# Kernel tuning notes

Measured on AMD Instinct MI355X. Metric: run time of the kernel, lower is better.

## Reference

```python
import jax, jax.numpy as jnp
import numpy as np

# --- static anchor geometry (exactly mirrors RPN._make_anchor_box) ---

def _valid_idx():
    scales = [64.0, 128.0, 256.0]
    ratios = [0.5, 1.0, 2.0]
    # (h, w) per anchor, normalized by 448
    anc = np.array([[s / np.sqrt(r), s * np.sqrt(r)] for s in scales for r in ratios]) / 448.0
    c = (np.arange(28) + 0.5) / 28.0
    cy = np.repeat(c, 28).reshape(28, 28)  # y varies along rows
    cx = np.tile(c, (28, 1))               # x varies along cols
    boxes = np.zeros((28, 28, 36))
    for a in range(9):
        boxes[..., 4 * a + 0] = cy
        boxes[..., 4 * a + 1] = cx
        boxes[..., 4 * a + 2] = anc[a, 0]
        boxes[..., 4 * a + 3] = anc[a, 1]
    b = boxes.reshape(-1, 4)  # [7056, 4] in yxhw
    y1 = b[:, 0] - b[:, 2] / 2
    x1 = b[:, 1] - b[:, 3] / 2
    y2 = b[:, 0] + b[:, 2] / 2
    x2 = b[:, 1] + b[:, 3] / 2
    return np.where((y1 > 0) & (x1 > 0) & (y2 < 28) & (x2 < 28))[0]

_VALID = _valid_idx()  # 4850 static indices

ROI_CLS_THRESHOLD = 0.9


def setup_inputs() -> dict:
    key = jax.random.key(0)
    ks = jax.random.split(key, 4)
    C = 2048
    return {
        'x': jax.random.normal(ks[0], (1, C, 28, 28), jnp.float32),
        'conv_w': jax.random.normal(ks[1], (C, C, 3, 3), jnp.float32) * 0.02,
        'conv_b': jnp.zeros((C,), jnp.float32),
        'reg_w': jax.random.normal(ks[2], (36, C), jnp.float32) * 0.02,
        'reg_b': jnp.zeros((36,), jnp.float32),
        'cls_w': jax.random.normal(ks[3], (9, C), jnp.float32) * 0.02,
        'cls_b': jnp.zeros((9,), jnp.float32),
    }


def reference(x, conv_w, conv_b, reg_w, reg_b, cls_w, cls_b):
    # Conv block: 3x3 conv + BatchNorm(identity at init: gamma=1, beta=0, running stats 0/1) + ReLU
    h = jax.lax.conv_general_dilated(
        x, conv_w, window_strides=(1, 1), padding=((1, 1), (1, 1)),
        dimension_numbers=('NCHW', 'OIHW', 'NCHW'))
    h = jax.nn.relu(h + conv_b[None, :, None, None])
    # 1x1 conv heads + sigmoid
    reg = jax.nn.sigmoid(jnp.einsum('bchw,oc->bohw', h, reg_w) + reg_b[None, :, None, None])  # [1,36,28,28]
    cls = jax.nn.sigmoid(jnp.einsum('bchw,oc->bohw', h, cls_w) + cls_b[None, :, None, None])  # [1,9,28,28]
    # exact replication of view/permute/squeeze + static valid-anchor gather
    reg = reg.reshape(1, 4, -1).transpose(0, 2, 1)[0][_VALID]  # [4850, 4]
    cls = cls.reshape(-1)[_VALID]                              # [4850]
    # inference path (gt=None): reg[cls > 0.9]; fixed-shape masked equivalent
    keep = cls > ROI_CLS_THRESHOLD
    return reg * keep[:, None]
```

## Files before the change

### kernel.cpp

```cpp
#include <hip/hip_runtime.h>
#include <cstdint>

typedef __attribute__((ext_vector_type(8))) short s8v;
typedef __attribute__((ext_vector_type(4))) float f4v;

__device__ __forceinline__ unsigned short bf16_rne(float f) {
    unsigned u = __float_as_uint(f);
    u += 0x7FFFu + ((u >> 16) & 1u);
    return (unsigned short)(u >> 16);
}
__device__ __forceinline__ float bf16f(unsigned short h) {
    return __uint_as_float(((unsigned)h) << 16);
}
__device__ __forceinline__ void cvt2(float a, float b, unsigned& hiw, unsigned& low) {
    unsigned ua = __float_as_uint(a), ub = __float_as_uint(b);
    unsigned ha = ua + 0x7FFFu + ((ua >> 16) & 1u);
    unsigned hb = ub + 0x7FFFu + ((ub >> 16) & 1u);
    hiw = (ha >> 16) | (hb & 0xFFFF0000u);
    float ra = a - __uint_as_float(ha & 0xFFFF0000u);
    float rb = b - __uint_as_float(hb & 0xFFFF0000u);
    unsigned la = __float_as_uint(ra), lb = __float_as_uint(rb);
    la += 0x7FFFu + ((la >> 16) & 1u);
    lb += 0x7FFFu + ((lb >> 16) & 1u);
    low = (la >> 16) | (lb & 0xFFFF0000u);
}
__device__ __forceinline__ void cvt2t(float a, float b, unsigned& hiw, unsigned& low) {
    unsigned ua = __float_as_uint(a), ub = __float_as_uint(b);
    hiw = (ua >> 16) | (ub & 0xFFFF0000u);
    float ra = a - __uint_as_float(ua & 0xFFFF0000u);
    float rb = b - __uint_as_float(ub & 0xFFFF0000u);
    unsigned la = __float_as_uint(ra), lb = __float_as_uint(rb);
    low = (la >> 16) | (lb & 0xFFFF0000u);
}

__global__ __launch_bounds__(256) void transpose_x(const float* __restrict__ x,
                                                   float* __restrict__ xt) {
    __shared__ float t[64][65];
    int c0 = blockIdx.x * 64, p0 = blockIdx.y * 64;
    int l = threadIdx.x & 63, g = threadIdx.x >> 6;
#pragma unroll
    for (int j = 0; j < 16; ++j) {
        int cc = j * 4 + g;
        int p = p0 + l;
        t[cc][l] = (p < 784) ? x[(size_t)(c0 + cc) * 784 + p] : 0.f;
    }
    __syncthreads();
#pragma unroll
    for (int j = 0; j < 16; ++j) {
        int pp = j * 4 + g;
        int p = p0 + pp;
        if (p < 784) xt[(size_t)p * 2048 + c0 + l] = t[l][pp];
    }
}

__global__ __launch_bounds__(256) void build_B(const float* __restrict__ xt,
                                               unsigned* __restrict__ Bhi,
                                               unsigned* __restrict__ Blo) {
    int p = blockIdx.x;
    int h = p / 28, w = p % 28;
#pragma unroll
    for (int it = 0; it < 4; ++it) {
        int cp = it * 256 + threadIdx.x;
        float va[18];
#pragma unroll
        for (int r = 0; r < 9; ++r) {
            int h2 = h + r / 3 - 1, w2 = w + r % 3 - 1;
            bool ok = (h2 >= 0) & (h2 < 28) & (w2 >= 0) & (w2 < 28);
            float2 v = ok ? ((const float2*)(xt + (size_t)(h2 * 28 + w2) * 2048))[cp]
                          : float2{0.f, 0.f};
            va[r] = v.x;
            va[9 + r] = v.y;
        }
        size_t base = (size_t)p * 9216 + (size_t)cp * 9;
#pragma unroll
        for (int d = 0; d < 9; ++d) {
            unsigned hw, lw;
            cvt2(va[2 * d], va[2 * d + 1], hw, lw);
            Bhi[base + d] = hw;
            Blo[base + d] = lw;
        }
    }
}

#define AHI_OFF 0
#define ALO_OFF 8192
#define BHI_OFF 16384
#define BLO_OFF 23552
#define LDS_BYTES 30720
#define KCH 1152
#define NSTEP 36

__global__ __launch_bounds__(256, 4) void conv_gemm(const float* __restrict__ cw,
                                                    const char* __restrict__ wsb,
                                                    uint32_t offBhi, uint32_t offBlo,
                                                    float* __restrict__ part) {
    __shared__ char smem[LDS_BYTES];
    int tid = threadIdx.x;
    int lane = tid & 63, wave = tid >> 6;
    int bm0 = blockIdx.x * 128, bn0 = blockIdx.y * 112, z = blockIdx.z;

    uint32_t doff[4], dlds[4];
#pragma unroll
    for (int j = 0; j < 4; ++j) {
        int i = j * 4 + wave;
        if (i >= 14) i -= 2;
        bool hiP = i < 7;
        int jj = hiP ? i : i - 7;
        int prow = jj * 16 + (lane >> 2);
        int pos = lane & 3;
        int gblk = pos ^ ((prow >> 1) & 3);
        uint32_t elem = (uint32_t)(bn0 + prow) * 18432 + (uint32_t)z * KCH + gblk * 8;
        doff[j] = (hiP ? offBhi : offBlo) + elem * 2;
        dlds[j] = (hiP ? BHI_OFF : BLO_OFF) + jj * 1024;
    }

    int m = lane & 15, qd = lane >> 4;
    int sw = (m >> 1) & 3;
    uint32_t apos = (uint32_t)(wave * 32 + m) * 64 + (uint32_t)((qd ^ sw) * 16);
    uint32_t bpos = (uint32_t)m * 64 + (uint32_t)((qd ^ sw) * 16);
    int arow = tid >> 1, ahalf = tid & 1;
    int swt = (arow >> 1) & 3;

    f4v acc[2][7];
#pragma unroll
    for (int a = 0; a < 2; ++a)
#pragma unroll
        for (int b = 0; b < 7; ++b) acc[a][b] = f4v{0.f, 0.f, 0.f, 0.f};

    const float4* ap = (const float4*)(cw + (size_t)(bm0 + arow) * 18432 + (size_t)z * KCH
                                       + (size_t)ahalf * 16);
    float4 arc[4], arn[4];
#pragma unroll
    for (int j = 0; j < 4; ++j) arc[j] = ap[j];

    for (int step = 0; step < NSTEP; ++step) {
#pragma unroll
        for (int j = 0; j < 4; ++j) {
            __builtin_amdgcn_global_load_lds(
                (const __attribute__((address_space(1))) void*)(wsb + doff[j]),
                (__attribute__((address_space(3))) void*)(smem + dlds[j]), 16, 0, 0);
            doff[j] += 64;
        }
        if (step < NSTEP - 1) {
            ap += 8;
#pragma unroll
            for (int j = 0; j < 4; ++j) arn[j] = ap[j];
        }
        unsigned hw[8], lw[8];
#pragma unroll
        for (int j = 0; j < 4; ++j) {
            cvt2t(arc[j].x, arc[j].y, hw[2 * j], lw[2 * j]);
            cvt2t(arc[j].z, arc[j].w, hw[2 * j + 1], lw[2 * j + 1]);
        }
#pragma unroll
        for (int b = 0; b < 2; ++b) {
            uint32_t col = (uint32_t)(((2 * ahalf + b) ^ swt) * 16);
            *(uint4*)(smem + AHI_OFF + arow * 64 + col) =
                uint4{hw[4 * b], hw[4 * b + 1], hw[4 * b + 2], hw[4 * b + 3]};
            *(uint4*)(smem + ALO_OFF + arow * 64 + col) =
                uint4{lw[4 * b], lw[4 * b + 1], lw[4 * b + 2], lw[4 * b + 3]};
        }
        __syncthreads();

        s8v ah[2], al[2];
#pragma unroll
        for (int mt = 0; mt < 2; ++mt) {
            ah[mt] = *(const s8v*)(smem + AHI_OFF + apos + mt * 1024);
            al[mt] = *(const s8v*)(smem + ALO_OFF + apos + mt * 1024);
        }
#pragma unroll
        for (int nt = 0; nt < 7; ++nt) {
            s8v bh = *(const s8v*)(smem + BHI_OFF + bpos + nt * 1024);
            s8v bl = *(const s8v*)(smem + BLO_OFF + bpos + nt * 1024);
#pragma unroll
            for (int mt = 0; mt < 2; ++mt) {
                acc[mt][nt] = __builtin_amdgcn_mfma_f32_16x16x32_bf16(ah[mt], bh, acc[mt][nt], 0, 0, 0);
                acc[mt][nt] = __builtin_amdgcn_mfma_f32_16x16x32_bf16(ah[mt], bl, acc[mt][nt], 0, 0, 0);
                acc[mt][nt] = __builtin_amdgcn_mfma_f32_16x16x32_bf16(al[mt], bh, acc[mt][nt], 0, 0, 0);
            }
        }
        __syncthreads();

        if (step < NSTEP - 1) {
#pragma unroll
            for (int j = 0; j < 4; ++j) arc[j] = arn[j];
        }
    }

    float* pz = part + (size_t)z * 1605632;
#pragma unroll
    for (int mt = 0; mt < 2; ++mt) {
        int o = bm0 + wave * 32 + mt * 16 + qd * 4;
#pragma unroll
        for (int nt = 0; nt < 7; ++nt) {
            int p = bn0 + nt * 16 + m;
            *(float4*)(pz + (size_t)p * 2048 + o) =
                float4{acc[mt][nt].x, acc[mt][nt].y, acc[mt][nt].z, acc[mt][nt].w};
        }
    }
}

__constant__ int HMIN_d[9] = {3, 2, 1, 6, 4, 3, 11, 8, 6};
__constant__ int WMIN_d[9] = {1, 2, 3, 3, 4, 6, 6, 8, 11};

__global__ __launch_bounds__(256) void heads(const float* __restrict__ part,
                                             const float* __restrict__ conv_b,
                                             const float* __restrict__ reg_w,
                                             const float* __restrict__ reg_b,
                                             const float* __restrict__ cls_w,
                                             const float* __restrict__ cls_b,
                                             float* __restrict__ out) {
    int tid = threadIdx.x;
    int lane = tid & 63, wave = tid >> 6;
    int p = blockIdx.x;
    int ci = tid * 2;

    float4 h0 = ((const float4*)conv_b)[ci];
    float4 h1 = ((const float4*)conv_b)[ci + 1];
#pragma unroll
    for (int z = 0; z < 16; ++z) {
        const float4* pz = (const float4*)(part + (size_t)z * 1605632 + (size_t)p * 2048);
        float4 a = pz[ci], b = pz[ci + 1];
        h0.x += a.x; h0.y += a.y; h0.z += a.z; h0.w += a.w;
        h1.x += b.x; h1.y += b.y; h1.z += b.z; h1.w += b.w;
    }
    h0.x = fmaxf(h0.x, 0.f); h0.y = fmaxf(h0.y, 0.f);
    h0.z = fmaxf(h0.z, 0.f); h0.w = fmaxf(h0.w, 0.f);
    h1.x = fmaxf(h1.x, 0.f); h1.y = fmaxf(h1.y, 0.f);
    h1.z = fmaxf(h1.z, 0.f); h1.w = fmaxf(h1.w, 0.f);

    float s[45];
#pragma unroll
    for (int o = 0; o < 36; ++o) {
        float4 wa = ((const float4*)(reg_w + (size_t)o * 2048))[ci];
        float4 wb = ((const float4*)(reg_w + (size_t)o * 2048))[ci + 1];
        s[o] = h0.x * wa.x + h0.y * wa.y + h0.z * wa.z + h0.w * wa.w +
               h1.x * wb.x + h1.y * wb.y + h1.z * wb.z + h1.w * wb.w;
    }
#pragma unroll
    for (int a = 0; a < 9; ++a) {
        float4 wa = ((const float4*)(cls_w + (size_t)a * 2048))[ci];
        float4 wb = ((const float4*)(cls_w + (size_t)a * 2048))[ci + 1];
        s[36 + a] = h0.x * wa.x + h0.y * wa.y + h0.z * wa.z + h0.w * wa.w +
                    h1.x * wb.x + h1.y * wb.y + h1.z * wb.z + h1.w * wb.w;
    }

    __shared__ float wsum[4][45];
    __shared__ float fin[45];
#pragma unroll
    for (int o = 0; o < 45; ++o) {
        float v = s[o];
#pragma unroll
        for (int d = 1; d < 64; d <<= 1) v += __shfl_xor(v, d, 64);
        if (lane == 0) wsum[wave][o] = v;
    }
    __syncthreads();
    if (tid < 45) fin[tid] = wsum[0][tid] + wsum[1][tid] + wsum[2][tid] + wsum[3][tid];
    __syncthreads();

    if (tid < 9) {
        int ap = tid;
        int n = ap * 784 + p;
        int pix = n / 9, a2 = n % 9;
        int hh = pix / 28, ww = pix % 28;
        if (hh >= HMIN_d[a2] && ww >= WMIN_d[a2]) {
            int row = 0;
#pragma unroll
            for (int a3 = 0; a3 < 9; ++a3) {
                int hm = HMIN_d[a3], wm = WMIN_d[a3];
                int full = hh - hm; if (full < 0) full = 0;
                row += full * (28 - wm);
                if (hh >= hm) { int prt = ww - wm; if (prt < 0) prt = 0; row += prt; }
                if (a3 < a2 && hh >= hm && ww >= wm) row += 1;
            }
            float cl = fin[36 + ap] + cls_b[ap];
            float keep = (1.f / (1.f + expf(-cl)) > 0.9f) ? 1.f : 0.f;
#pragma unroll
            for (int q = 0; q < 4; ++q) {
                float rl = fin[q * 9 + ap] + reg_b[q * 9 + ap];
                out[row * 4 + q] = keep / (1.f + expf(-rl));
            }
        }
    }
}

extern "C" void kernel_launch(void* const* d_in, const int* in_sizes, int n_in,
                              void* d_out, int out_size, void* d_ws, size_t ws_size,
                              hipStream_t stream) {
    const float* x = (const float*)d_in[0];
    const float* conv_w = (const float*)d_in[1];
    const float* conv_b = (const float*)d_in[2];
    const float* reg_w = (const float*)d_in[3];
    const float* reg_b = (const float*)d_in[4];
    const float* cls_w = (const float*)d_in[5];
    const float* cls_b = (const float*)d_in[6];
    float* out = (float*)d_out;
    char* ws = (char*)d_ws;

    const size_t o_part = 0;
    const size_t o_xt = 0;
    const size_t o_Bhi = 102760448;
    const size_t o_Blo = 131661824;

    transpose_x<<<dim3(32, 13), 256, 0, stream>>>(x, (float*)(ws + o_xt));
    build_B<<<784, 256, 0, stream>>>((const float*)(ws + o_xt), (unsigned*)(ws + o_Bhi),
                                     (unsigned*)(ws + o_Blo));
    conv_gemm<<<dim3(16, 7, 16), 256, 0, stream>>>(conv_w, ws, (uint32_t)o_Bhi,
                                                   (uint32_t)o_Blo, (float*)(ws + o_part));
    heads<<<784, 256, 0, stream>>>((const float*)(ws + o_part), conv_b, reg_w, reg_b,
                                   cls_w, cls_b, out);
}
```

Measured before the change: 487.8 us.

## Stage build_B output in LDS for coalesced stores and drop duplicate B-tile loads

build_B now writes its bf16 hi/lo pairs into a shared-memory staging buffer and then emits wide, contiguous uint4 stores to global memory. Before, each thread wrote 9 strided words per plane. In conv_gemm, the 14 B-tile load slices are spread across the 4 waves as 4/4/3/3, which removes the duplicated loads of slices 12 and 13. The launch-bounds occupancy hint rises from 4 to 6 blocks per SM, which may force fewer registers per thread and risk spills. The 36 KB shared buffer in build_B limits how many of its blocks can run at once.

```diff
diff --git a/kernel.cpp b/kernel.cpp
--- a/kernel.cpp
+++ b/kernel.cpp
@@ -56,29 +56,42 @@
 __global__ __launch_bounds__(256) void build_B(const float* __restrict__ xt,
                                                unsigned* __restrict__ Bhi,
                                                unsigned* __restrict__ Blo) {
-    int p = blockIdx.x;
+    __shared__ unsigned stage[9216];
+    int p = blockIdx.x, tid = threadIdx.x;
     int h = p / 28, w = p % 28;
-#pragma unroll
-    for (int it = 0; it < 4; ++it) {
-        int cp = it * 256 + threadIdx.x;
-        float va[18];
-#pragma unroll
-        for (int r = 0; r < 9; ++r) {
-            int h2 = h + r / 3 - 1, w2 = w + r % 3 - 1;
-            bool ok = (h2 >= 0) & (h2 < 28) & (w2 >= 0) & (w2 < 28);
-            float2 v = ok ? ((const float2*)(xt + (size_t)(h2 * 28 + w2) * 2048))[cp]
-                          : float2{0.f, 0.f};
-            va[r] = v.x;
-            va[9 + r] = v.y;
-        }
-        size_t base = (size_t)p * 9216 + (size_t)cp * 9;
-#pragma unroll
-        for (int d = 0; d < 9; ++d) {
-            unsigned hw, lw;
-            cvt2(va[2 * d], va[2 * d + 1], hw, lw);
-            Bhi[base + d] = hw;
-            Blo[base + d] = lw;
-        }
+    for (int half = 0; half < 2; ++half) {
+#pragma unroll
+        for (int il = 0; il < 2; ++il) {
+            int cpl = il * 256 + tid;
+            int cpg = half * 512 + cpl;
+            float va[18];
+#pragma unroll
+            for (int r = 0; r < 9; ++r) {
+                int h2 = h + r / 3 - 1, w2 = w + r % 3 - 1;
+                bool ok = (h2 >= 0) & (h2 < 28) & (w2 >= 0) & (w2 < 28);
+                float2 v = ok ? ((const float2*)(xt + (size_t)(h2 * 28 + w2) * 2048))[cpg]
+                              : float2{0.f, 0.f};
+                va[r] = v.x;
+                va[9 + r] = v.y;
+            }
+#pragma unroll
+            for (int d = 0; d < 9; ++d) {
+                unsigned hwd, lwd;
+                cvt2(va[2 * d], va[2 * d + 1], hwd, lwd);
+                stage[cpl * 9 + d] = hwd;
+                stage[4608 + cpl * 9 + d] = lwd;
+            }
+        }
+        __syncthreads();
+        size_t rowbase = (size_t)p * 9216 + (size_t)half * 4608;
+#pragma unroll
+        for (int j = 0; j < 9; ++j) {
+            int idx = j * 1024 + tid * 4;
+            uint4 v = *(const uint4*)&stage[idx];
+            if (idx < 4608) *(uint4*)&Bhi[rowbase + idx] = v;
+            else            *(uint4*)&Blo[rowbase + (idx - 4608)] = v;
+        }
+        __syncthreads();
     }
 }
 
@@ -90,7 +103,7 @@
 #define KCH 1152
 #define NSTEP 36
 
-__global__ __launch_bounds__(256, 4) void conv_gemm(const float* __restrict__ cw,
+__global__ __launch_bounds__(256, 6) void conv_gemm(const float* __restrict__ cw,
                                                     const char* __restrict__ wsb,
                                                     uint32_t offBhi, uint32_t offBlo,
                                                     float* __restrict__ part) {
@@ -99,11 +112,13 @@
     int lane = tid & 63, wave = tid >> 6;
     int bm0 = blockIdx.x * 128, bn0 = blockIdx.y * 112, z = blockIdx.z;
 
+    int nj = (wave < 2) ? 4 : 3;
+    int ibase = (wave < 2) ? wave * 4 : 8 + (wave - 2) * 3;
     uint32_t doff[4], dlds[4];
 #pragma unroll
     for (int j = 0; j < 4; ++j) {
-        int i = j * 4 + wave;
-        if (i >= 14) i -= 2;
+        int i = ibase + j;
+        if (i > 13) i = 13;
         bool hiP = i < 7;
         int jj = hiP ? i : i - 7;
         int prow = jj * 16 + (lane >> 2);
@@ -136,10 +151,12 @@
     for (int step = 0; step < NSTEP; ++step) {
 #pragma unroll
         for (int j = 0; j < 4; ++j) {
-            __builtin_amdgcn_global_load_lds(
-                (const __attribute__((address_space(1))) void*)(wsb + doff[j]),
-                (__attribute__((address_space(3))) void*)(smem + dlds[j]), 16, 0, 0);
-            doff[j] += 64;
+            if (j < nj) {
+                __builtin_amdgcn_global_load_lds(
+                    (const __attribute__((address_space(1))) void*)(wsb + doff[j]),
+                    (__attribute__((address_space(3))) void*)(smem + dlds[j]), 16, 0, 0);
+                doff[j] += 64;
+            }
         }
         if (step < NSTEP - 1) {
             ap += 8;
```

Result: slower. 498.0 us (+2.1%).
